# Optimization experiments

Hardware: AMD Instinct MI355X
Metric: run time of the kernel (lower is better)

## Reference

```python
import jax, jax.numpy as jnp
import numpy as np

BN_EPS = 1e-5


def conv1x1(x, W, b):
    # x: [B, Cin, N], W: [Cout, Cin], b: [Cout]
    return jnp.einsum('oc,bcn->bon', W, x) + b[None, :, None]


def bn(x, p):
    # p: [4, C] rows = gamma, beta, running_mean, running_var (inference BN)
    g, be, m, v = p[0], p[1], p[2], p[3]
    inv = jax.lax.rsqrt(v + BN_EPS)
    return (x - m[None, :, None]) * (g * inv)[None, :, None] + be[None, :, None]


def conv_bn_relu(x, W, b, p):
    return jax.nn.relu(bn(conv1x1(x, W, b), p))


def _make_params(key, cout, cin):
    k1, k2 = jax.random.split(key)
    W = jax.random.normal(k1, (cout, cin), jnp.float32) * (1.0 / np.sqrt(cin))
    b = jax.random.normal(k2, (cout,), jnp.float32) * 0.01
    p = jnp.stack([jnp.ones(cout), jnp.zeros(cout), jnp.zeros(cout), jnp.ones(cout)]).astype(jnp.float32)
    return W, b, p


def setup_inputs() -> dict:
    key = jax.random.key(0)
    ks = jax.random.split(key, 16)
    B, N, S, D1, D2 = 2, 16384, 4096, 128, 256
    Cin, C, Cm = D1 + D2 + 13, 128, 128  # 397, out_channel, mlp[0]
    inp = {
        'xyz1': jax.random.normal(ks[0], (B, N, 3), jnp.float32),
        'xyz2': jax.random.normal(ks[1], (B, S, 3), jnp.float32),
        'points1': jax.random.normal(ks[2], (B, D1, N), jnp.float32),
        'points2': jax.random.normal(ks[3], (B, D2, S), jnp.float32),
        'last_pred': jax.random.normal(ks[4], (B, S, 13), jnp.float32),
    }
    inp['fuse_W'], inp['fuse_b'], inp['fuse_bn'] = _make_params(ks[5], C, Cin)
    inp['ext1_W'], inp['ext1_b'], inp['ext1_bn'] = _make_params(ks[6], C, C)
    inp['ext2_W'], inp['ext2_b'], inp['ext2_bn'] = _make_params(ks[7], C, C)
    inp['pred1_W'], inp['pred1_b'], inp['pred1_bn'] = _make_params(ks[8], Cm, C)
    inp['pred2_W'], inp['pred2_b'], inp['pred2_bn'] = _make_params(ks[9], 13, Cm)
    return inp


def _forward(xyz1, xyz2, points1, points2, last_pred,
             fuse_W, fuse_b, fuse_bn, ext1_W, ext1_b, ext1_bn,
             ext2_W, ext2_b, ext2_bn, pred1_W, pred1_b, pred1_bn,
             pred2_W, pred2_b, pred2_bn):
    B, N, _ = xyz1.shape
    p1 = jnp.transpose(points1, (0, 2, 1))  # [B, N, D1]
    p2 = jnp.transpose(points2, (0, 2, 1))  # [B, S, D2]
    # squared distances [B, N, S]
    dists = (jnp.sum(xyz1 ** 2, -1)[:, :, None]
             + jnp.sum(xyz2 ** 2, -1)[:, None, :]
             - 2.0 * jnp.einsum('bnc,bsc->bns', xyz1, xyz2))
    # 3 smallest distances (partial top-k instead of full sort; same math)
    neg_d3, idx = jax.lax.top_k(-dists, 3)  # [B, N, 3]
    d3 = -neg_d3
    recip = 1.0 / (d3 + 1e-8)
    weight = recip / jnp.sum(recip, axis=2, keepdims=True)  # [B, N, 3]
    bidx = jnp.arange(B)[:, None, None]
    interp_pts = jnp.sum(p2[bidx, idx] * weight[..., None], axis=2)        # [B, N, D2]
    interp_pred = jnp.sum(last_pred[bidx, idx] * weight[..., None], axis=2)  # [B, N, 13]
    new_points = jnp.transpose(jnp.concatenate([p1, interp_pts, interp_pred], axis=-1), (0, 2, 1))  # [B, Cin, N]
    # fuse
    x = conv_bn_relu(new_points, fuse_W, fuse_b, fuse_bn)
    # extraction: one ConvBNReLURes1D block (groups=1, res_expansion=1)
    h = conv_bn_relu(x, ext1_W, ext1_b, ext1_bn)
    x = jax.nn.relu(bn(conv1x1(h, ext2_W, ext2_b), ext2_bn) + x)  # [B, C, N]
    new_points_out = x
    # prediction head (dropout is identity in eval mode)
    feat = conv_bn_relu(x, pred1_W, pred1_b, pred1_bn)
    pred = conv_bn_relu(feat, pred2_W, pred2_b, pred2_bn)
    return (new_points_out,
            jnp.transpose(feat, (0, 2, 1)),
            jnp.transpose(pred, (0, 2, 1)))


def reference(xyz1, xyz2, points1, points2, last_pred,
              fuse_W, fuse_b, fuse_bn, ext1_W, ext1_b, ext1_bn,
              ext2_W, ext2_b, ext2_bn, pred1_W, pred1_b, pred1_bn,
              pred2_W, pred2_b, pred2_bn):
    return _forward(xyz1, xyz2, points1, points2, last_pred,
                    fuse_W, fuse_b, fuse_bn, ext1_W, ext1_b, ext1_bn,
                    ext2_W, ext2_b, ext2_bn, pred1_W, pred1_b, pred1_bn,
                    pred2_W, pred2_b, pred2_bn)
```

## Files before the change

### kernel.cpp

```cpp
#include <hip/hip_runtime.h>
#include <stdint.h>

#define B_   2
#define N_   16384
#define S_   4096
#define D2_  256
#define CIN_ 397
#define KP_  416
#define C_   128
#define OC_  13
#define NCHUNK_ 8
#define CHS_ (S_ / NCHUNK_)

typedef unsigned short u16;
typedef unsigned int u32;
typedef short s16x8 __attribute__((ext_vector_type(8)));
typedef float f32x4 __attribute__((ext_vector_type(4)));

#define MFMA16(a, b, c) __builtin_amdgcn_mfma_f32_16x16x32_bf16((a), (b), (c), 0, 0, 0)

__device__ __forceinline__ float b2f(u16 h) {
  union { unsigned int u; float f; } v; v.u = ((unsigned int)h) << 16; return v.f;
}
__device__ __forceinline__ u16 f2b(float f) {
  union { float f; unsigned int u; } v; v.f = f;
  unsigned int r = v.u + 0x7fffu + ((v.u >> 16) & 1u);
  return (u16)(r >> 16);
}

__global__ void prep_kernel(const float* __restrict__ fW, const float* __restrict__ fb,
                            const float* __restrict__ fbn,
                            const float* __restrict__ e1W, const float* __restrict__ e1b,
                            const float* __restrict__ e1bn,
                            const float* __restrict__ e2W, const float* __restrict__ e2b,
                            const float* __restrict__ e2bn,
                            const float* __restrict__ p1W, const float* __restrict__ p1b,
                            const float* __restrict__ p1bn,
                            const float* __restrict__ p2W, const float* __restrict__ p2b,
                            const float* __restrict__ p2bn,
                            u16* __restrict__ Wf, u16* __restrict__ W1o,
                            u16* __restrict__ W2o, u16* __restrict__ W3o,
                            u16* __restrict__ Wp2, float* __restrict__ st) {
  int tid = blockIdx.x * 256 + threadIdx.x;
  int stride = gridDim.x * 256;
  for (int i = tid; i < 128 * KP_; i += stride) {
    int m = i / KP_, k = i - m * KP_;
    Wf[i] = (k < CIN_) ? f2b(fW[m * CIN_ + k]) : (u16)0;
  }
  for (int i = tid; i < 128 * 128; i += stride) {
    W1o[i] = f2b(e1W[i]);
    W2o[i] = f2b(e2W[i]);
    W3o[i] = f2b(p1W[i]);
  }
  for (int i = tid; i < 16 * 128; i += stride) {
    int m = i >> 7;
    Wp2[i] = (m < OC_) ? f2b(p2W[i]) : (u16)0;
  }
  for (int i = tid; i < 5 * 128; i += stride) {
    int sg = i >> 7, c = i & 127;
    const float* bn; const float* bc; int Cc = 128;
    switch (sg) {
      case 0: bn = fbn;  bc = fb;  break;
      case 1: bn = e1bn; bc = e1b; break;
      case 2: bn = e2bn; bc = e2b; break;
      case 3: bn = p1bn; bc = p1b; break;
      default: bn = p2bn; bc = p2b; Cc = OC_; break;
    }
    float s = 0.f, t = 0.f;
    if (c < Cc) {
      float g  = bn[0 * Cc + c], be = bn[1 * Cc + c];
      float mu = bn[2 * Cc + c], vv = bn[3 * Cc + c];
      float inv = 1.0f / sqrtf(vv + 1e-5f);
      s = g * inv;
      t = (bc[c] - mu) * s + be;
    }
    st[sg * 256 + c] = s;
    st[sg * 256 + 128 + c] = t;
  }
}

__global__ void transpose_f2b_kernel(const float* __restrict__ in, u16* __restrict__ out,
                                     int C, int S, int opitch) {
  __shared__ float tile[64][65];
  int b = blockIdx.z;
  int s0 = blockIdx.x * 64, c0 = blockIdx.y * 64;
  const float* ip = in + (size_t)b * C * S;
  u16* op = out + (size_t)b * S * opitch;
  int tr = threadIdx.x >> 4;
  int tc4 = (threadIdx.x & 15) * 4;
#pragma unroll
  for (int r = 0; r < 64; r += 16) {
    float4 v = *(const float4*)(ip + (size_t)(c0 + tr + r) * S + s0 + tc4);
    tile[tr + r][tc4 + 0] = v.x;
    tile[tr + r][tc4 + 1] = v.y;
    tile[tr + r][tc4 + 2] = v.z;
    tile[tr + r][tc4 + 3] = v.w;
  }
  __syncthreads();
#pragma unroll
  for (int r = 0; r < 64; r += 16) {
    ushort4 v;
    v.x = f2b(tile[tc4 + 0][tr + r]);
    v.y = f2b(tile[tc4 + 1][tr + r]);
    v.z = f2b(tile[tc4 + 2][tr + r]);
    v.w = f2b(tile[tc4 + 3][tr + r]);
    *(ushort4*)(op + (size_t)(s0 + tr + r) * opitch + c0 + tc4) = v;
  }
}

__global__ __launch_bounds__(256) void knn_scan_kernel(
    const float* __restrict__ xyz1, const float* __restrict__ xyz2,
    u16* __restrict__ cand) {
  __shared__ float4 pts[CHS_];
  int b = blockIdx.z;
  int chunk = blockIdx.x;
  int s0 = chunk * CHS_;
  int tid = threadIdx.x;
  const float* x2 = xyz2 + ((size_t)b * S_ + s0) * 3;
  for (int i = tid; i < CHS_; i += 256) {
    float xx = x2[i * 3], yy = x2[i * 3 + 1], zz = x2[i * 3 + 2];
    pts[i] = make_float4(xx, yy, zz, fmaf(xx, xx, fmaf(yy, yy, zz * zz)));
  }
  __syncthreads();
  int n = blockIdx.y * 256 + tid;
  const float* x1 = xyz1 + ((size_t)b * N_ + n) * 3;
  float ax = x1[0], ay = x1[1], az = x1[2];
  float n1 = fmaf(ax, ax, fmaf(ay, ay, az * az));
  u32 k0 = 0xFFFFFFFFu, k1 = 0xFFFFFFFFu, k2 = 0xFFFFFFFFu, k3 = 0xFFFFFFFFu;
#pragma unroll 8
  for (int s = 0; s < CHS_; ++s) {
    float4 p = pts[s];
    float dot = fmaf(ax, p.x, fmaf(ay, p.y, az * p.z));
    float d = fmaf(-2.f, dot, n1 + p.w);
    d = fmaxf(d, 0.f);
    u32 key = (__float_as_uint(d) & 0xFFFFF000u) | (u32)(s0 + s);
    u32 nk0 = min(k0, key);
    u32 nk1 = min(k1, max(k0, key));
    u32 nk2 = min(k2, max(k1, key));
    u32 nk3 = min(k3, max(k2, key));
    k0 = nk0; k1 = nk1; k2 = nk2; k3 = nk3;
  }
  u16* co = cand + ((size_t)(b * N_ + n)) * (NCHUNK_ * 4) + chunk * 4;
  co[0] = (u16)(k0 & 0xFFFu);
  co[1] = (u16)(k1 & 0xFFFu);
  co[2] = (u16)(k2 & 0xFFFu);
  co[3] = (u16)(k3 & 0xFFFu);
}

__global__ void knn_merge_kernel(const float* __restrict__ xyz1,
                                 const float* __restrict__ xyz2,
                                 const u16* __restrict__ cand,
                                 float* __restrict__ wout, int* __restrict__ iout) {
#pragma clang fp contract(off)
  int q = blockIdx.x * 256 + threadIdx.x;
  int b = q >> 14;
  const u16* ci = cand + (size_t)q * (NCHUNK_ * 4);
  const float* x1 = xyz1 + (size_t)q * 3;
  double ax = x1[0], ay = x1[1], az = x1[2];
  double n1 = (ax * ax + ay * ay) + az * az;
  const float* x2b = xyz2 + (size_t)b * S_ * 3;
  double D0 = 1e300, D1 = 1e300, D2v = 1e300;
  int I0 = 2147483647, I1 = 2147483647, I2 = 2147483647;
  for (int j = 0; j < NCHUNK_ * 4; ++j) {
    int i = ci[j];
    const float* p = x2b + (size_t)i * 3;
    double px = p[0], py = p[1], pz = p[2];
    double n2 = (px * px + py * py) + pz * pz;
    double dot = (ax * px + ay * py) + az * pz;
    double d = (n1 + n2) - 2.0 * dot;
    if ((d < D2v) || (d == D2v && i < I2)) {
      if ((d < D1) || (d == D1 && i < I1)) {
        D2v = D1; I2 = I1;
        if ((d < D0) || (d == D0 && i < I0)) { D1 = D0; I1 = I0; D0 = d; I0 = i; }
        else                                  { D1 = d; I1 = i; }
      } else { D2v = d; I2 = i; }
    }
  }
  double r0 = 1.0 / (D0 + 1e-8);
  double r1 = 1.0 / (D1 + 1e-8);
  double r2 = 1.0 / (D2v + 1e-8);
  double sum = (r0 + r1) + r2;
  size_t o = (size_t)q * 3;
  wout[o + 0] = (float)(r0 / sum);
  wout[o + 1] = (float)(r1 / sum);
  wout[o + 2] = (float)(r2 / sum);
  iout[o + 0] = I0; iout[o + 1] = I1; iout[o + 2] = I2;
}

__global__ void interp_kernel(const u16* __restrict__ p2t, const float* __restrict__ last_pred,
                              const float* __restrict__ knw, const int* __restrict__ kni,
                              u16* __restrict__ npT) {
#pragma clang fp contract(off)
  int b = blockIdx.y;
  int n = blockIdx.x * 4 + (threadIdx.x >> 6);
  int lane = threadIdx.x & 63;
  size_t o = ((size_t)b * N_ + n) * 3;
  float w0 = knw[o], w1 = knw[o + 1], w2 = knw[o + 2];
  int i0 = kni[o], i1 = kni[o + 1], i2 = kni[o + 2];
  const u16* r0 = p2t + ((size_t)b * S_ + i0) * D2_;
  const u16* r1 = p2t + ((size_t)b * S_ + i1) * D2_;
  const u16* r2 = p2t + ((size_t)b * S_ + i2) * D2_;
  u16* orow = npT + ((size_t)b * N_ + n) * KP_;
  ushort4 a0 = *(const ushort4*)(r0 + lane * 4);
  ushort4 a1 = *(const ushort4*)(r1 + lane * 4);
  ushort4 a2 = *(const ushort4*)(r2 + lane * 4);
  ushort4 v;
  v.x = f2b((w0 * b2f(a0.x) + w1 * b2f(a1.x)) + w2 * b2f(a2.x));
  v.y = f2b((w0 * b2f(a0.y) + w1 * b2f(a1.y)) + w2 * b2f(a2.y));
  v.z = f2b((w0 * b2f(a0.z) + w1 * b2f(a1.z)) + w2 * b2f(a2.z));
  v.w = f2b((w0 * b2f(a0.w) + w1 * b2f(a1.w)) + w2 * b2f(a2.w));
  *(ushort4*)(orow + 128 + lane * 4) = v;
  const float* lp = last_pred + (size_t)b * S_ * OC_;
  if (lane < OC_) {
    float v2 = (w0 * lp[i0 * OC_ + lane] + w1 * lp[i1 * OC_ + lane])
               + w2 * lp[i2 * OC_ + lane];
    orow[384 + lane] = f2b(v2);
  }
  if (lane < KP_ - CIN_) orow[CIN_ + lane] = 0;
}

__device__ __forceinline__ void gemm_lds128(const u16* __restrict__ W, const u16* xb,
                                            int l15, int lq, int nbase, f32x4 acc[8][2]) {
#pragma unroll
  for (int mt = 0; mt < 8; ++mt) {
    acc[mt][0] = (f32x4){0.f, 0.f, 0.f, 0.f};
    acc[mt][1] = (f32x4){0.f, 0.f, 0.f, 0.f};
  }
  for (int ks = 0; ks < 4; ++ks) {
    int ko = ks * 32 + lq * 8;
    s16x8 b0 = *(const s16x8*)(xb + (nbase + l15) * 136 + ko);
    s16x8 b1 = *(const s16x8*)(xb + (nbase + 16 + l15) * 136 + ko);
#pragma unroll
    for (int mt = 0; mt < 8; ++mt) {
      s16x8 a = *(const s16x8*)(W + (size_t)(mt * 16 + l15) * 128 + ko);
      acc[mt][0] = MFMA16(a, b0, acc[mt][0]);
      acc[mt][1] = MFMA16(a, b1, acc[mt][1]);
    }
  }
}

__global__ __launch_bounds__(256) void mega_kernel(
    const u16* __restrict__ npT, const u16* __restrict__ Wf,
    const u16* __restrict__ W1, const u16* __restrict__ W2,
    const u16* __restrict__ W3, const u16* __restrict__ Wp2,
    const float* __restrict__ st, float* __restrict__ out) {
  __shared__ u16 xb0[128 * 136];
  __shared__ u16 xb1[128 * 136];
  int b = blockIdx.y;
  int n0 = blockIdx.x * 128;
  int tid = threadIdx.x;
  int wv = tid >> 6, lane = tid & 63;
  int l15 = lane & 15, lq = lane >> 4;
  int nbase = wv * 32;
  f32x4 acc[8][2];

#pragma unroll
  for (int mt = 0; mt < 8; ++mt) {
    acc[mt][0] = (f32x4){0.f, 0.f, 0.f, 0.f};
    acc[mt][1] = (f32x4){0.f, 0.f, 0.f, 0.f};
  }
  {
    const u16* brow0 = npT + ((size_t)(b * N_ + n0 + nbase + l15)) * KP_;
    const u16* brow1 = brow0 + (size_t)16 * KP_;
#pragma unroll 1
    for (int ks = 0; ks < KP_ / 32; ++ks) {
      int ko = ks * 32 + lq * 8;
      s16x8 bf0 = *(const s16x8*)(brow0 + ko);
      s16x8 bf1 = *(const s16x8*)(brow1 + ko);
#pragma unroll
      for (int mt = 0; mt < 8; ++mt) {
        s16x8 a = *(const s16x8*)(Wf + (size_t)(mt * 16 + l15) * KP_ + ko);
        acc[mt][0] = MFMA16(a, bf0, acc[mt][0]);
        acc[mt][1] = MFMA16(a, bf1, acc[mt][1]);
      }
    }
  }
#pragma unroll
  for (int mt = 0; mt < 8; ++mt) {
    f32x4 sc = *(const f32x4*)(st + 0 * 256 + mt * 16 + lq * 4);
    f32x4 bi = *(const f32x4*)(st + 0 * 256 + 128 + mt * 16 + lq * 4);
#pragma unroll
    for (int nt = 0; nt < 2; ++nt) {
      int n_l = nbase + nt * 16 + l15;
      ushort4 v;
      v.x = f2b(fmaxf(acc[mt][nt][0] * sc[0] + bi[0], 0.f));
      v.y = f2b(fmaxf(acc[mt][nt][1] * sc[1] + bi[1], 0.f));
      v.z = f2b(fmaxf(acc[mt][nt][2] * sc[2] + bi[2], 0.f));
      v.w = f2b(fmaxf(acc[mt][nt][3] * sc[3] + bi[3], 0.f));
      *(ushort4*)(&xb0[n_l * 136 + mt * 16 + lq * 4]) = v;
    }
  }
  __syncthreads();

  gemm_lds128(W1, xb0, l15, lq, nbase, acc);
#pragma unroll
  for (int mt = 0; mt < 8; ++mt) {
    f32x4 sc = *(const f32x4*)(st + 1 * 256 + mt * 16 + lq * 4);
    f32x4 bi = *(const f32x4*)(st + 1 * 256 + 128 + mt * 16 + lq * 4);
#pragma unroll
    for (int nt = 0; nt < 2; ++nt) {
      int n_l = nbase + nt * 16 + l15;
      ushort4 v;
      v.x = f2b(fmaxf(acc[mt][nt][0] * sc[0] + bi[0], 0.f));
      v.y = f2b(fmaxf(acc[mt][nt][1] * sc[1] + bi[1], 0.f));
      v.z = f2b(fmaxf(acc[mt][nt][2] * sc[2] + bi[2], 0.f));
      v.w = f2b(fmaxf(acc[mt][nt][3] * sc[3] + bi[3], 0.f));
      *(ushort4*)(&xb1[n_l * 136 + mt * 16 + lq * 4]) = v;
    }
  }
  __syncthreads();

  gemm_lds128(W2, xb1, l15, lq, nbase, acc);
#pragma unroll
  for (int mt = 0; mt < 8; ++mt) {
    f32x4 sc = *(const f32x4*)(st + 2 * 256 + mt * 16 + lq * 4);
    f32x4 bi = *(const f32x4*)(st + 2 * 256 + 128 + mt * 16 + lq * 4);
#pragma unroll
    for (int nt = 0; nt < 2; ++nt) {
      int n_l = nbase + nt * 16 + l15;
      int n_g = n0 + n_l;
      ushort4 xp = *(const ushort4*)(&xb0[n_l * 136 + mt * 16 + lq * 4]);
      float v0 = fmaxf(acc[mt][nt][0] * sc[0] + bi[0] + b2f(xp.x), 0.f);
      float v1 = fmaxf(acc[mt][nt][1] * sc[1] + bi[1] + b2f(xp.y), 0.f);
      float v2 = fmaxf(acc[mt][nt][2] * sc[2] + bi[2] + b2f(xp.z), 0.f);
      float v3 = fmaxf(acc[mt][nt][3] * sc[3] + bi[3] + b2f(xp.w), 0.f);
      ushort4 v;
      v.x = f2b(v0); v.y = f2b(v1); v.z = f2b(v2); v.w = f2b(v3);
      *(ushort4*)(&xb0[n_l * 136 + mt * 16 + lq * 4]) = v;
      int m = mt * 16 + lq * 4;
      out[((size_t)(b * C_ + m + 0)) * N_ + n_g] = v0;
      out[((size_t)(b * C_ + m + 1)) * N_ + n_g] = v1;
      out[((size_t)(b * C_ + m + 2)) * N_ + n_g] = v2;
      out[((size_t)(b * C_ + m + 3)) * N_ + n_g] = v3;
    }
  }
  __syncthreads();

  gemm_lds128(W3, xb0, l15, lq, nbase, acc);
  {
    float* out1 = out + (size_t)B_ * C_ * N_;
#pragma unroll
    for (int mt = 0; mt < 8; ++mt) {
      f32x4 sc = *(const f32x4*)(st + 3 * 256 + mt * 16 + lq * 4);
      f32x4 bi = *(const f32x4*)(st + 3 * 256 + 128 + mt * 16 + lq * 4);
#pragma unroll
      for (int nt = 0; nt < 2; ++nt) {
        int n_l = nbase + nt * 16 + l15;
        int n_g = n0 + n_l;
        float v0 = fmaxf(acc[mt][nt][0] * sc[0] + bi[0], 0.f);
        float v1 = fmaxf(acc[mt][nt][1] * sc[1] + bi[1], 0.f);
        float v2 = fmaxf(acc[mt][nt][2] * sc[2] + bi[2], 0.f);
        float v3 = fmaxf(acc[mt][nt][3] * sc[3] + bi[3], 0.f);
        ushort4 v;
        v.x = f2b(v0); v.y = f2b(v1); v.z = f2b(v2); v.w = f2b(v3);
        *(ushort4*)(&xb1[n_l * 136 + mt * 16 + lq * 4]) = v;
        float4 o4 = make_float4(v0, v1, v2, v3);
        *(float4*)(out1 + ((size_t)(b * N_ + n_g)) * 128 + mt * 16 + lq * 4) = o4;
      }
    }
  }
  __syncthreads();

  {
    f32x4 a2[2];
    a2[0] = (f32x4){0.f, 0.f, 0.f, 0.f};
    a2[1] = (f32x4){0.f, 0.f, 0.f, 0.f};
    for (int ks = 0; ks < 4; ++ks) {
      int ko = ks * 32 + lq * 8;
      s16x8 b0 = *(const s16x8*)(&xb1[(nbase + l15) * 136 + ko]);
      s16x8 b1 = *(const s16x8*)(&xb1[(nbase + 16 + l15) * 136 + ko]);
      s16x8 a = *(const s16x8*)(Wp2 + (size_t)l15 * 128 + ko);
      a2[0] = MFMA16(a, b0, a2[0]);
      a2[1] = MFMA16(a, b1, a2[1]);
    }
    float* out2 = out + (size_t)B_ * C_ * N_ + (size_t)B_ * N_ * 128;
    f32x4 sc = *(const f32x4*)(st + 4 * 256 + lq * 4);
    f32x4 bi = *(const f32x4*)(st + 4 * 256 + 128 + lq * 4);
#pragma unroll
    for (int nt = 0; nt < 2; ++nt) {
      int n_g = n0 + nbase + nt * 16 + l15;
#pragma unroll
      for (int r = 0; r < 4; ++r) {
        int m = lq * 4 + r;
        if (m < OC_) {
          out2[((size_t)(b * N_ + n_g)) * OC_ + m] =
              fmaxf(a2[nt][r] * sc[r] + bi[r], 0.f);
        }
      }
    }
  }
}

extern "C" void kernel_launch(void* const* d_in, const int* in_sizes, int n_in,
                              void* d_out, int out_size, void* d_ws, size_t ws_size,
                              hipStream_t stream) {
  const float* xyz1      = (const float*)d_in[0];
  const float* xyz2      = (const float*)d_in[1];
  const float* points1   = (const float*)d_in[2];
  const float* points2   = (const float*)d_in[3];
  const float* last_pred = (const float*)d_in[4];
  const float* fuse_W    = (const float*)d_in[5];
  const float* fuse_b    = (const float*)d_in[6];
  const float* fuse_bn   = (const float*)d_in[7];
  const float* ext1_W    = (const float*)d_in[8];
  const float* ext1_b    = (const float*)d_in[9];
  const float* ext1_bn   = (const float*)d_in[10];
  const float* ext2_W    = (const float*)d_in[11];
  const float* ext2_b    = (const float*)d_in[12];
  const float* ext2_bn   = (const float*)d_in[13];
  const float* pred1_W   = (const float*)d_in[14];
  const float* pred1_b   = (const float*)d_in[15];
  const float* pred1_bn  = (const float*)d_in[16];
  const float* pred2_W   = (const float*)d_in[17];
  const float* pred2_b   = (const float*)d_in[18];
  const float* pred2_bn  = (const float*)d_in[19];

  char* ws = (char*)d_ws;
  u16*   npT  = (u16*)(ws + 0);
  u16*   p2t  = (u16*)(ws + 27262976);
  float* knw  = (float*)(ws + 31457280);
  int*   kni  = (int*)(ws + 31850496);
  u16*   cand = (u16*)(ws + 32243712);
  u16*   Wf   = (u16*)(ws + 34340864);
  u16*   W1   = (u16*)(ws + 34447360);
  u16*   W2   = (u16*)(ws + 34480128);
  u16*   W3   = (u16*)(ws + 34512896);
  u16*   Wp2  = (u16*)(ws + 34545664);
  float* st   = (float*)(ws + 34549760);

  prep_kernel<<<dim3(64), dim3(256), 0, stream>>>(
      fuse_W, fuse_b, fuse_bn, ext1_W, ext1_b, ext1_bn, ext2_W, ext2_b, ext2_bn,
      pred1_W, pred1_b, pred1_bn, pred2_W, pred2_b, pred2_bn,
      Wf, W1, W2, W3, Wp2, st);

  transpose_f2b_kernel<<<dim3(N_ / 64, 128 / 64, B_), dim3(256), 0, stream>>>(
      points1, npT, 128, N_, KP_);
  transpose_f2b_kernel<<<dim3(S_ / 64, 256 / 64, B_), dim3(256), 0, stream>>>(
      points2, p2t, 256, S_, 256);

  knn_scan_kernel<<<dim3(NCHUNK_, N_ / 256, B_), dim3(256), 0, stream>>>(
      xyz1, xyz2, cand);
  knn_merge_kernel<<<dim3(B_ * N_ / 256), dim3(256), 0, stream>>>(
      xyz1, xyz2, cand, knw, kni);

  interp_kernel<<<dim3(N_ / 4, B_), dim3(256), 0, stream>>>(
      p2t, last_pred, knw, kni, npT);

  mega_kernel<<<dim3(N_ / 128, B_), dim3(256), 0, stream>>>(
      npT, Wf, W1, W2, W3, Wp2, st, (float*)d_out);
}
```

Before: 231.7 us.

## Fuse interpolation into mega kernel via LDS and rebalance KNN chunk scan

```diff
diff --git a/kernel.cpp b/kernel.cpp
--- a/kernel.cpp
+++ b/kernel.cpp
@@ -9,8 +9,10 @@
 #define KP_  416
 #define C_   128
 #define OC_  13
-#define NCHUNK_ 8
+#define NCHUNK_ 16
 #define CHS_ (S_ / NCHUNK_)
+#define NCAND_ (NCHUNK_ * 3)
+#define XBI_P 296
 
 typedef unsigned short u16;
 typedef unsigned int u32;
@@ -117,34 +119,32 @@
   int s0 = chunk * CHS_;
   int tid = threadIdx.x;
   const float* x2 = xyz2 + ((size_t)b * S_ + s0) * 3;
-  for (int i = tid; i < CHS_; i += 256) {
-    float xx = x2[i * 3], yy = x2[i * 3 + 1], zz = x2[i * 3 + 2];
-    pts[i] = make_float4(xx, yy, zz, fmaf(xx, xx, fmaf(yy, yy, zz * zz)));
+  {
+    float xx = x2[tid * 3], yy = x2[tid * 3 + 1], zz = x2[tid * 3 + 2];
+    pts[tid] = make_float4(xx, yy, zz, fmaf(xx, xx, fmaf(yy, yy, zz * zz)));
   }
   __syncthreads();
   int n = blockIdx.y * 256 + tid;
   const float* x1 = xyz1 + ((size_t)b * N_ + n) * 3;
   float ax = x1[0], ay = x1[1], az = x1[2];
   float n1 = fmaf(ax, ax, fmaf(ay, ay, az * az));
-  u32 k0 = 0xFFFFFFFFu, k1 = 0xFFFFFFFFu, k2 = 0xFFFFFFFFu, k3 = 0xFFFFFFFFu;
+  u32 k0 = 0xFFFFFFFFu, k1 = 0xFFFFFFFFu, k2 = 0xFFFFFFFFu;
 #pragma unroll 8
   for (int s = 0; s < CHS_; ++s) {
     float4 p = pts[s];
     float dot = fmaf(ax, p.x, fmaf(ay, p.y, az * p.z));
     float d = fmaf(-2.f, dot, n1 + p.w);
     d = fmaxf(d, 0.f);
-    u32 key = (__float_as_uint(d) & 0xFFFFF000u) | (u32)(s0 + s);
+    u32 key = (__float_as_uint(d) & 0xFFFFFF00u) | (u32)s;
     u32 nk0 = min(k0, key);
     u32 nk1 = min(k1, max(k0, key));
     u32 nk2 = min(k2, max(k1, key));
-    u32 nk3 = min(k3, max(k2, key));
-    k0 = nk0; k1 = nk1; k2 = nk2; k3 = nk3;
-  }
-  u16* co = cand + ((size_t)(b * N_ + n)) * (NCHUNK_ * 4) + chunk * 4;
-  co[0] = (u16)(k0 & 0xFFFu);
-  co[1] = (u16)(k1 & 0xFFFu);
-  co[2] = (u16)(k2 & 0xFFFu);
-  co[3] = (u16)(k3 & 0xFFFu);
+    k0 = nk0; k1 = nk1; k2 = nk2;
+  }
+  u16* co = cand + ((size_t)(b * N_ + n)) * NCAND_ + chunk * 3;
+  co[0] = (u16)((k0 & 0xFFu) + s0);
+  co[1] = (u16)((k1 & 0xFFu) + s0);
+  co[2] = (u16)((k2 & 0xFFu) + s0);
 }
 
 __global__ void knn_merge_kernel(const float* __restrict__ xyz1,
@@ -154,14 +154,14 @@
 #pragma clang fp contract(off)
   int q = blockIdx.x * 256 + threadIdx.x;
   int b = q >> 14;
-  const u16* ci = cand + (size_t)q * (NCHUNK_ * 4);
+  const u16* ci = cand + (size_t)q * NCAND_;
   const float* x1 = xyz1 + (size_t)q * 3;
   double ax = x1[0], ay = x1[1], az = x1[2];
   double n1 = (ax * ax + ay * ay) + az * az;
   const float* x2b = xyz2 + (size_t)b * S_ * 3;
   double D0 = 1e300, D1 = 1e300, D2v = 1e300;
   int I0 = 2147483647, I1 = 2147483647, I2 = 2147483647;
-  for (int j = 0; j < NCHUNK_ * 4; ++j) {
+  for (int j = 0; j < NCAND_; ++j) {
     int i = ci[j];
     const float* p = x2b + (size_t)i * 3;
     double px = p[0], py = p[1], pz = p[2];
@@ -187,38 +187,6 @@
   iout[o + 0] = I0; iout[o + 1] = I1; iout[o + 2] = I2;
 }
 
-__global__ void interp_kernel(const u16* __restrict__ p2t, const float* __restrict__ last_pred,
-                              const float* __restrict__ knw, const int* __restrict__ kni,
-                              u16* __restrict__ npT) {
-#pragma clang fp contract(off)
-  int b = blockIdx.y;
-  int n = blockIdx.x * 4 + (threadIdx.x >> 6);
-  int lane = threadIdx.x & 63;
-  size_t o = ((size_t)b * N_ + n) * 3;
-  float w0 = knw[o], w1 = knw[o + 1], w2 = knw[o + 2];
-  int i0 = kni[o], i1 = kni[o + 1], i2 = kni[o + 2];
-  const u16* r0 = p2t + ((size_t)b * S_ + i0) * D2_;
-  const u16* r1 = p2t + ((size_t)b * S_ + i1) * D2_;
-  const u16* r2 = p2t + ((size_t)b * S_ + i2) * D2_;
-  u16* orow = npT + ((size_t)b * N_ + n) * KP_;
-  ushort4 a0 = *(const ushort4*)(r0 + lane * 4);
-  ushort4 a1 = *(const ushort4*)(r1 + lane * 4);
-  ushort4 a2 = *(const ushort4*)(r2 + lane * 4);
-  ushort4 v;
-  v.x = f2b((w0 * b2f(a0.x) + w1 * b2f(a1.x)) + w2 * b2f(a2.x));
-  v.y = f2b((w0 * b2f(a0.y) + w1 * b2f(a1.y)) + w2 * b2f(a2.y));
-  v.z = f2b((w0 * b2f(a0.z) + w1 * b2f(a1.z)) + w2 * b2f(a2.z));
-  v.w = f2b((w0 * b2f(a0.w) + w1 * b2f(a1.w)) + w2 * b2f(a2.w));
-  *(ushort4*)(orow + 128 + lane * 4) = v;
-  const float* lp = last_pred + (size_t)b * S_ * OC_;
-  if (lane < OC_) {
-    float v2 = (w0 * lp[i0 * OC_ + lane] + w1 * lp[i1 * OC_ + lane])
-               + w2 * lp[i2 * OC_ + lane];
-    orow[384 + lane] = f2b(v2);
-  }
-  if (lane < KP_ - CIN_) orow[CIN_ + lane] = 0;
-}
-
 __device__ __forceinline__ void gemm_lds128(const u16* __restrict__ W, const u16* xb,
                                             int l15, int lq, int nbase, f32x4 acc[8][2]) {
 #pragma unroll
@@ -240,12 +208,16 @@
 }
 
 __global__ __launch_bounds__(256) void mega_kernel(
-    const u16* __restrict__ npT, const u16* __restrict__ Wf,
+    const u16* __restrict__ npT, const u16* __restrict__ p2t,
+    const float* __restrict__ last_pred,
+    const float* __restrict__ knw, const int* __restrict__ kni,
+    const u16* __restrict__ Wf,
     const u16* __restrict__ W1, const u16* __restrict__ W2,
     const u16* __restrict__ W3, const u16* __restrict__ Wp2,
     const float* __restrict__ st, float* __restrict__ out) {
   __shared__ u16 xb0[128 * 136];
   __shared__ u16 xb1[128 * 136];
+  __shared__ u16 xbi[128 * XBI_P];
   int b = blockIdx.y;
   int n0 = blockIdx.x * 128;
   int tid = threadIdx.x;
@@ -254,22 +226,63 @@
   int nbase = wv * 32;
   f32x4 acc[8][2];
 
+  {
+    const float* lpb = last_pred + (size_t)b * S_ * OC_;
+    const u16* p2b = p2t + (size_t)b * S_ * D2_;
+#pragma unroll 1
+    for (int i = 0; i < 32; ++i) {
+      int p = nbase + i;
+      size_t o = ((size_t)(b * N_ + n0 + p)) * 3;
+      float w0 = knw[o], w1 = knw[o + 1], w2 = knw[o + 2];
+      int i0 = kni[o], i1 = kni[o + 1], i2 = kni[o + 2];
+      ushort4 a0 = *(const ushort4*)(p2b + (size_t)i0 * D2_ + lane * 4);
+      ushort4 a1 = *(const ushort4*)(p2b + (size_t)i1 * D2_ + lane * 4);
+      ushort4 a2 = *(const ushort4*)(p2b + (size_t)i2 * D2_ + lane * 4);
+      ushort4 v;
+      v.x = f2b((w0 * b2f(a0.x) + w1 * b2f(a1.x)) + w2 * b2f(a2.x));
+      v.y = f2b((w0 * b2f(a0.y) + w1 * b2f(a1.y)) + w2 * b2f(a2.y));
+      v.z = f2b((w0 * b2f(a0.z) + w1 * b2f(a1.z)) + w2 * b2f(a2.z));
+      v.w = f2b((w0 * b2f(a0.w) + w1 * b2f(a1.w)) + w2 * b2f(a2.w));
+      *(ushort4*)(&xbi[p * XBI_P + lane * 4]) = v;
+      if (lane < 32) {
+        u16 pv = 0;
+        if (lane < OC_) {
+          pv = f2b((w0 * lpb[i0 * OC_ + lane] + w1 * lpb[i1 * OC_ + lane])
+                   + w2 * lpb[i2 * OC_ + lane]);
+        }
+        xbi[p * XBI_P + 256 + lane] = pv;
+      }
+    }
+  }
+
 #pragma unroll
   for (int mt = 0; mt < 8; ++mt) {
     acc[mt][0] = (f32x4){0.f, 0.f, 0.f, 0.f};
     acc[mt][1] = (f32x4){0.f, 0.f, 0.f, 0.f};
   }
   {
-    const u16* brow0 = npT + ((size_t)(b * N_ + n0 + nbase + l15)) * KP_;
-    const u16* brow1 = brow0 + (size_t)16 * KP_;
+    const u16* brow0 = npT + ((size_t)(b * N_ + n0 + nbase + l15)) * 128;
+    const u16* brow1 = brow0 + (size_t)16 * 128;
 #pragma unroll 1
-    for (int ks = 0; ks < KP_ / 32; ++ks) {
+    for (int ks = 0; ks < 4; ++ks) {
       int ko = ks * 32 + lq * 8;
       s16x8 bf0 = *(const s16x8*)(brow0 + ko);
       s16x8 bf1 = *(const s16x8*)(brow1 + ko);
 #pragma unroll
       for (int mt = 0; mt < 8; ++mt) {
         s16x8 a = *(const s16x8*)(Wf + (size_t)(mt * 16 + l15) * KP_ + ko);
+        acc[mt][0] = MFMA16(a, bf0, acc[mt][0]);
+        acc[mt][1] = MFMA16(a, bf1, acc[mt][1]);
+      }
+    }
+#pragma unroll 1
+    for (int ks = 0; ks < 9; ++ks) {
+      int kk = ks * 32 + lq * 8;
+      s16x8 bf0 = *(const s16x8*)(&xbi[(nbase + l15) * XBI_P + kk]);
+      s16x8 bf1 = *(const s16x8*)(&xbi[(nbase + 16 + l15) * XBI_P + kk]);
+#pragma unroll
+      for (int mt = 0; mt < 8; ++mt) {
+        s16x8 a = *(const s16x8*)(Wf + (size_t)(mt * 16 + l15) * KP_ + 128 + kk);
         acc[mt][0] = MFMA16(a, bf0, acc[mt][0]);
         acc[mt][1] = MFMA16(a, bf1, acc[mt][1]);
       }
@@ -417,16 +430,16 @@
 
   char* ws = (char*)d_ws;
   u16*   npT  = (u16*)(ws + 0);
-  u16*   p2t  = (u16*)(ws + 27262976);
-  float* knw  = (float*)(ws + 31457280);
-  int*   kni  = (int*)(ws + 31850496);
-  u16*   cand = (u16*)(ws + 32243712);
-  u16*   Wf   = (u16*)(ws + 34340864);
-  u16*   W1   = (u16*)(ws + 34447360);
-  u16*   W2   = (u16*)(ws + 34480128);
-  u16*   W3   = (u16*)(ws + 34512896);
-  u16*   Wp2  = (u16*)(ws + 34545664);
-  float* st   = (float*)(ws + 34549760);
+  u16*   p2t  = (u16*)(ws + 8388608);
+  float* knw  = (float*)(ws + 12582912);
+  int*   kni  = (int*)(ws + 12976128);
+  u16*   cand = (u16*)(ws + 13369344);
+  u16*   Wf   = (u16*)(ws + 16515072);
+  u16*   W1   = (u16*)(ws + 16621568);
+  u16*   W2   = (u16*)(ws + 16654336);
+  u16*   W3   = (u16*)(ws + 16687104);
+  u16*   Wp2  = (u16*)(ws + 16719872);
+  float* st   = (float*)(ws + 16723968);
 
   prep_kernel<<<dim3(64), dim3(256), 0, stream>>>(
       fuse_W, fuse_b, fuse_bn, ext1_W, ext1_b, ext1_bn, ext2_W, ext2_b, ext2_bn,
@@ -434,7 +447,7 @@
       Wf, W1, W2, W3, Wp2, st);
 
   transpose_f2b_kernel<<<dim3(N_ / 64, 128 / 64, B_), dim3(256), 0, stream>>>(
-      points1, npT, 128, N_, KP_);
+      points1, npT, 128, N_, 128);
   transpose_f2b_kernel<<<dim3(S_ / 64, 256 / 64, B_), dim3(256), 0, stream>>>(
       points2, p2t, 256, S_, 256);
 
@@ -443,9 +456,6 @@
   knn_merge_kernel<<<dim3(B_ * N_ / 256), dim3(256), 0, stream>>>(
       xyz1, xyz2, cand, knw, kni);
 
-  interp_kernel<<<dim3(N_ / 4, B_), dim3(256), 0, stream>>>(
-      p2t, last_pred, knw, kni, npT);
-
   mega_kernel<<<dim3(N_ / 128, B_), dim3(256), 0, stream>>>(
-      npT, Wf, W1, W2, W3, Wp2, st, (float*)d_out);
-}
+      npT, p2t, last_pred, knw, kni, Wf, W1, W2, W3, Wp2, st, (float*)d_out);
+}
```

Result: slower. 238.2 us (+2.8%).
